# Performance work log

Measured on AMD Instinct MI355X. Metric: run time of the kernel, lower is better.

The kernel has to match this reference:

```python
import jax, jax.numpy as jnp
import numpy as np

E, T, DIN, DOUT = 8, 32768, 1024, 4096


def setup_inputs() -> dict:
    key = jax.random.key(0)
    k1, k2, k3 = jax.random.split(key, 3)
    input = jax.random.normal(k1, (T, DIN), dtype=jnp.float32)
    weight = jax.random.normal(k2, (E, DOUT, DIN), dtype=jnp.float32) * 0.02
    bias = jax.random.normal(k3, (E, DOUT), dtype=jnp.float32) * 0.02
    # balanced routing: 4096 tokens per expert, sums to T
    num_experts_per_token = jnp.full((E,), T // E, dtype=jnp.int64)
    return {"input": input, "weight": weight, "bias": bias,
            "num_experts_per_token": num_experts_per_token}


def reference(input, weight, bias, num_experts_per_token):
    # counts are routing metadata -> static (mirrors .tolist() in torch)
    counts = np.asarray(num_experts_per_token)
    offsets = np.concatenate([[0], np.cumsum(counts)])  # [E+1]
    num_experts = weight.shape[0]
    outs = []
    for i in range(num_experts):  # fixed small loop over experts (grouped GEMM)
        xi = input[offsets[i]:offsets[i + 1]]          # [n_i, DIN]
        yi = xi @ weight[i].T + bias[i]                # [n_i, DOUT]
        outs.append(yi)
    return jnp.concatenate(outs, axis=0)               # [T, DOUT]
```

## Files before the change

kernel.cpp:

```cpp
#include <hip/hip_runtime.h>
#include <hip/hip_bf16.h>


#define DEVFN __device__ __forceinline__

constexpr int E_    = 8;
constexpr int T_    = 32768;
constexpr int DIN_  = 1024;
constexpr int DOUT_ = 4096;

typedef __attribute__((ext_vector_type(8))) __bf16 bf16x8;
typedef __attribute__((ext_vector_type(4))) float  f32x4;
typedef __attribute__((ext_vector_type(8))) short  s16x8;

DEVFN unsigned short f2bf(float x) {
  unsigned u = __builtin_bit_cast(unsigned, x);
  u += 0x7fffu + ((u >> 16) & 1u);
  return (unsigned short)(u >> 16);
}

DEVFN long long expert_offset(const void* cnts, int e) {
  const int* c32 = (const int*)cnts;
  long long s = 0;
  for (int i = 0; i < E_; ++i) s += c32[i];
  if (s == (long long)T_) {
    long long o = 0;
    for (int i = 0; i < e; ++i) o += c32[i];
    return o;
  }
  const long long* c64 = (const long long*)cnts;
  long long o = 0;
  for (int i = 0; i < e; ++i) o += c64[i];
  return o;
}

__global__ __launch_bounds__(256) void cvt2_kernel(const float* __restrict__ ia,
                                                   const float* __restrict__ iw,
                                                   unsigned short* __restrict__ oa,
                                                   unsigned short* __restrict__ ow,
                                                   int nA4, int nW4) {
  int i = blockIdx.x * 256 + threadIdx.x;
  const float* src;
  unsigned short* dst;
  int j;
  if (i < nA4) { src = ia; dst = oa; j = i; }
  else         { j = i - nA4; if (j >= nW4) return; src = iw; dst = ow; }
  const float4 f = reinterpret_cast<const float4*>(src)[j];
  ushort4 h;
  h.x = f2bf(f.x); h.y = f2bf(f.y); h.z = f2bf(f.z); h.w = f2bf(f.w);
  reinterpret_cast<ushort4*>(dst)[j] = h;
}

__global__ __launch_bounds__(512, 2) void gemm5_kernel(const unsigned short* __restrict__ wa,
                                                       const unsigned short* __restrict__ wb,
                                                       const float* __restrict__ bias,
                                                       const void* __restrict__ counts,
                                                       float* __restrict__ out) {
  __shared__ __align__(16) unsigned char lds[2][2][32768];

  const int tid  = threadIdx.x;
  const int lane = tid & 63;
  const int wid  = tid >> 6;
  const int wm = wid >> 2, wn = wid & 3;

  const int p = blockIdx.x;
  const int e = p & 7;
  const int q = p >> 3;

  const long long off = expert_offset(counts, e);
  const unsigned short* wae = wa + off * (long long)DIN_;
  const unsigned short* wbe = wb + (long long)e * DOUT_ * DIN_;
  const float* be = bias + e * DOUT_;

  int goff[4];
#pragma unroll
  for (int rd = 0; rd < 4; ++rd) {
    const int chunk = rd * 512 + tid;
    const int r = chunk >> 3, c = chunk & 7;
    goff[rd] = r * DIN_ + ((c ^ (r & 7)) << 3);
  }
  auto stage = [&](const unsigned short* g, unsigned char* l) {
#pragma unroll
    for (int rd = 0; rd < 4; ++rd)
      __builtin_amdgcn_global_load_lds(
          (const __attribute__((address_space(1))) void*)(g + goff[rd]),
          (__attribute__((address_space(3))) void*)(l + (rd * 512 + tid) * 16), 16, 0, 0);
  };

  const int rsel = lane & 15, hi = lane >> 4;
  int lp[2];
  lp[0] = rsel * 128 + (((hi)     ^ (rsel & 7)) << 4);
  lp[1] = rsel * 128 + (((4 + hi) ^ (rsel & 7)) << 4);
  const int abase = wm * 128 * 128;
  const int bbase = wn * 64 * 128;

  bf16x8 a[4][2];
  bf16x8 b[2][2][2];
  f32x4  acc[8][4];

  auto quad = [&](int am0, int qn) {
#pragma unroll
    for (int mf = 0; mf < 4; ++mf)
#pragma unroll
      for (int j = 0; j < 2; ++j)
#pragma unroll
        for (int kk = 0; kk < 2; ++kk)
          acc[am0 + mf][qn * 2 + j] = __builtin_amdgcn_mfma_f32_16x16x32_bf16(
              a[mf][kk], b[qn][j][kk], acc[am0 + mf][qn * 2 + j], 0, 0, 0);
  };

  int tm = q >> 3, tn = q & 7;
  const unsigned short* wat = wae + (long long)tm * 256 * DIN_;
  const unsigned short* wbt = wbe + (long long)tn * 256 * DIN_;
  stage(wat,      &lds[0][0][0]);
  stage(wbt,      &lds[0][1][0]);
  stage(wat + 64, &lds[1][0][0]);
  stage(wbt + 64, &lds[1][1][0]);
  asm volatile("s_waitcnt vmcnt(8)" ::: "memory");
  __builtin_amdgcn_s_barrier();

  for (int it = 0; it < 8; ++it) {
    const int ocol0 = tn * 256 + wn * 64;
    {
      const float bv0 = be[ocol0 + rsel];
      const float bv1 = be[ocol0 + 16 + rsel];
      const float bv2 = be[ocol0 + 32 + rsel];
      const float bv3 = be[ocol0 + 48 + rsel];
#pragma unroll
      for (int am = 0; am < 8; ++am) {
        acc[am][0] = (f32x4){bv0, bv0, bv0, bv0};
        acc[am][1] = (f32x4){bv1, bv1, bv1, bv1};
        acc[am][2] = (f32x4){bv2, bv2, bv2, bv2};
        acc[am][3] = (f32x4){bv3, bv3, bv3, bv3};
      }
    }
    const bool have_next = (it < 7);
    int ntm = tm, ntn = tn;
    if (have_next) { ntm = ((it + 1) & 3) * 4 + (q >> 3); ntn = ((it + 1) >> 2) * 8 + (q & 7); }
    const unsigned short* nat = wae + (long long)ntm * 256 * DIN_;
    const unsigned short* nbt = wbe + (long long)ntn * 256 * DIN_;

    for (int kt = 0; kt < 16; ++kt) {
      unsigned char* Ab = &lds[kt & 1][0][0];
      unsigned char* Bb = &lds[kt & 1][1][0];
      const unsigned short* pfa = nullptr;
      const unsigned short* pfb = nullptr;
      int nend = -1;
      if (kt < 14)        { pfa = wat + (kt + 2) * 64; pfb = wbt + (kt + 2) * 64; nend = 8; }
      else if (have_next) { pfa = nat + (kt - 14) * 64; pfb = nbt + (kt - 14) * 64; nend = 8; }
      else if (kt == 14)  { nend = 0; }

#pragma unroll
      for (int mf = 0; mf < 4; ++mf) {
        a[mf][0] = *(const bf16x8*)(Ab + abase + mf * 2048 + lp[0]);
        a[mf][1] = *(const bf16x8*)(Ab + abase + mf * 2048 + lp[1]);
      }
#pragma unroll
      for (int j = 0; j < 2; ++j) {
        b[0][j][0] = *(const bf16x8*)(Bb + bbase + j * 2048 + lp[0]);
        b[0][j][1] = *(const bf16x8*)(Bb + bbase + j * 2048 + lp[1]);
      }
      __builtin_amdgcn_s_setprio(1); quad(0, 0); __builtin_amdgcn_s_setprio(0);
#pragma unroll
      for (int j = 0; j < 2; ++j) {
        b[1][j][0] = *(const bf16x8*)(Bb + bbase + 4096 + j * 2048 + lp[0]);
        b[1][j][1] = *(const bf16x8*)(Bb + bbase + 4096 + j * 2048 + lp[1]);
      }
      __builtin_amdgcn_s_setprio(1); quad(0, 1); __builtin_amdgcn_s_setprio(0);
#pragma unroll
      for (int mf = 0; mf < 4; ++mf) {
        a[mf][0] = *(const bf16x8*)(Ab + abase + 8192 + mf * 2048 + lp[0]);
        a[mf][1] = *(const bf16x8*)(Ab + abase + 8192 + mf * 2048 + lp[1]);
      }
      __builtin_amdgcn_s_setprio(1); quad(4, 1); __builtin_amdgcn_s_setprio(0);
      __builtin_amdgcn_s_barrier();

      if (pfb) stage(pfb, Bb);
      if (pfa) stage(pfa, Ab);
      __builtin_amdgcn_sched_barrier(0);
      __builtin_amdgcn_s_setprio(1); quad(4, 0); __builtin_amdgcn_s_setprio(0);
      if (nend == 8)      asm volatile("s_waitcnt vmcnt(8)" ::: "memory");
      else if (nend == 0) asm volatile("s_waitcnt vmcnt(0)" ::: "memory");
      __builtin_amdgcn_s_barrier();
    }

    const long long orow0 = off + (long long)tm * 256 + wm * 128;
#pragma unroll
    for (int am = 0; am < 8; ++am) {
      const int rl = (am >> 2) * 64 + (am & 3) * 16 + hi * 4;
#pragma unroll
      for (int j = 0; j < 4; ++j) {
        float* rp = out + (orow0 + rl + j) * (long long)DOUT_ + ocol0 + rsel;
        rp[0]  = acc[am][0][j];
        rp[16] = acc[am][1][j];
        rp[32] = acc[am][2][j];
        rp[48] = acc[am][3][j];
      }
    }
    wat = nat; wbt = nbt; tm = ntm; tn = ntn;
  }
}

__global__ __launch_bounds__(256) void gemm_fb_kernel(const float* __restrict__ Af,
                                                      const float* __restrict__ Bf,
                                                      const float* __restrict__ bias,
                                                      const void* __restrict__ counts,
                                                      float* __restrict__ out) {
  constexpr int RS = 144;
  constexpr int BBASE = 128 * RS;
  __shared__ __align__(16) unsigned char lds[2 * 128 * RS];

  const int tid  = threadIdx.x;
  const int lane = tid & 63;
  const int wid  = tid >> 6;
  const int wm = wid >> 1, wn = wid & 1;

  const int bid = blockIdx.x;
  const int e  = bid >> 10;
  const int t  = bid & 1023;
  const int tm = t >> 5, tn = t & 31;

  const long long off = expert_offset(counts, e);
  const long long rowA0 = off + (long long)tm * 128;
  const int n0 = tn * 128;

  f32x4 acc[4][4] = {};

  for (int kt = 0; kt < DIN_ / 64; ++kt) {
    const int k0 = kt * 64;
#pragma unroll
    for (int rd = 0; rd < 8; ++rd) {
      const int chunk = rd * 256 + tid;
      const int c2 = chunk & 1023;
      const int r  = c2 >> 3;
      const int c  = c2 & 7;
      const float* src =
          (rd < 4) ? (Af + (rowA0 + r) * (long long)DIN_ + (k0 + c * 8))
                   : (Bf + ((long long)(e * DOUT_ + n0 + r)) * DIN_ + (k0 + c * 8));
      const float4 f0 = *reinterpret_cast<const float4*>(src);
      const float4 f1 = *reinterpret_cast<const float4*>(src + 4);
      s16x8 v;
      v[0] = (short)f2bf(f0.x); v[1] = (short)f2bf(f0.y);
      v[2] = (short)f2bf(f0.z); v[3] = (short)f2bf(f0.w);
      v[4] = (short)f2bf(f1.x); v[5] = (short)f2bf(f1.y);
      v[6] = (short)f2bf(f1.z); v[7] = (short)f2bf(f1.w);
      *reinterpret_cast<s16x8*>(&lds[((rd < 4) ? 0 : BBASE) + r * RS + (c << 4)]) = v;
    }
    __syncthreads();
#pragma unroll
    for (int kk = 0; kk < 2; ++kk) {
      const int rs = lane & 15;
      const int cs = kk * 4 + (lane >> 4);
      bf16x8 af[4], bfr[4];
#pragma unroll
      for (int mf = 0; mf < 4; ++mf)
        af[mf] = *reinterpret_cast<const bf16x8*>(&lds[(wm * 64 + mf * 16 + rs) * RS + (cs << 4)]);
#pragma unroll
      for (int nf = 0; nf < 4; ++nf)
        bfr[nf] = *reinterpret_cast<const bf16x8*>(&lds[BBASE + (wn * 64 + nf * 16 + rs) * RS + (cs << 4)]);
#pragma unroll
      for (int mf = 0; mf < 4; ++mf)
#pragma unroll
        for (int nf = 0; nf < 4; ++nf)
          acc[mf][nf] = __builtin_amdgcn_mfma_f32_16x16x32_bf16(af[mf], bfr[nf], acc[mf][nf], 0, 0, 0);
    }
    __syncthreads();
  }

  const long long orow0 = off + (long long)tm * 128 + wm * 64;
  const int ocol0 = n0 + wn * 64;
  const int rlo = (lane >> 4) * 4;
  const int c15 = lane & 15;
#pragma unroll
  for (int nf = 0; nf < 4; ++nf) {
    const int n = ocol0 + nf * 16 + c15;
    const float bv = bias[e * DOUT_ + n];
#pragma unroll
    for (int mf = 0; mf < 4; ++mf) {
      const long long mrow = orow0 + mf * 16 + rlo;
#pragma unroll
      for (int j = 0; j < 4; ++j)
        out[(mrow + j) * (long long)DOUT_ + n] = acc[mf][nf][j] + bv;
    }
  }
}

extern "C" void kernel_launch(void* const* d_in, const int* in_sizes, int n_in,
                              void* d_out, int out_size, void* d_ws, size_t ws_size,
                              hipStream_t stream) {
  const float* input  = (const float*)d_in[0];
  const float* weight = (const float*)d_in[1];
  const float* bias   = (const float*)d_in[2];
  const void*  counts = (const void*)d_in[3];
  float* out = (float*)d_out;

  const size_t nA = (size_t)T_ * DIN_;
  const size_t nW = (size_t)E_ * DOUT_ * DIN_;
  const size_t need = (nA + nW) * sizeof(unsigned short);

  if (ws_size >= need) {
    unsigned short* wa = (unsigned short*)d_ws;
    unsigned short* wb = wa + nA;
    const int nA4 = (int)(nA / 4), nW4 = (int)(nW / 4);
    cvt2_kernel<<<dim3((unsigned)((nA4 + nW4) / 256)), dim3(256), 0, stream>>>(
        input, weight, wa, wb, nA4, nW4);
    gemm5_kernel<<<dim3(256), dim3(512), 0, stream>>>(wa, wb, bias, counts, out);
  } else {
    gemm_fb_kernel<<<dim3(E_ * 32 * 32), dim3(256), 0, stream>>>(input, weight, bias, counts, out);
  }
}
```

Before: 385.6 us.

## Load B fragments directly from global memory instead of staging through LDS

The weight (B) tile is no longer staged into shared memory. Each lane now loads its MFMA B fragments straight from global memory, and only the A tile is double-buffered through LDS. This halves LDS usage and staging traffic per block, which could allow more occupancy and fewer LDS reads. The cost is that B loads now go uncoalesced across lanes, hitting a 16-row by 16-byte pattern, and each B element is re-read by the two wm warps. These loads also sit on the critical path with no prefetch, and the vmcnt waits now count these extra loads, which may add stalls.

Measured after the change: 550.5 us. 42.8% more time.

```diff
diff --git a/kernel.cpp b/kernel.cpp
--- a/kernel.cpp
+++ b/kernel.cpp
@@ -51,12 +51,12 @@
   reinterpret_cast<ushort4*>(dst)[j] = h;
 }
 
-__global__ __launch_bounds__(512, 2) void gemm5_kernel(const unsigned short* __restrict__ wa,
+__global__ __launch_bounds__(512, 2) void gemm6_kernel(const unsigned short* __restrict__ wa,
                                                        const unsigned short* __restrict__ wb,
                                                        const float* __restrict__ bias,
                                                        const void* __restrict__ counts,
                                                        float* __restrict__ out) {
-  __shared__ __align__(16) unsigned char lds[2][2][32768];
+  __shared__ __align__(16) unsigned char lds[2][32768];
 
   const int tid  = threadIdx.x;
   const int lane = tid & 63;
@@ -79,7 +79,7 @@
     const int r = chunk >> 3, c = chunk & 7;
     goff[rd] = r * DIN_ + ((c ^ (r & 7)) << 3);
   }
-  auto stage = [&](const unsigned short* g, unsigned char* l) {
+  auto stageA = [&](const unsigned short* g, unsigned char* l) {
 #pragma unroll
     for (int rd = 0; rd < 4; ++rd)
       __builtin_amdgcn_global_load_lds(
@@ -92,7 +92,6 @@
   lp[0] = rsel * 128 + (((hi)     ^ (rsel & 7)) << 4);
   lp[1] = rsel * 128 + (((4 + hi) ^ (rsel & 7)) << 4);
   const int abase = wm * 128 * 128;
-  const int bbase = wn * 64 * 128;
 
   bf16x8 a[4][2];
   bf16x8 b[2][2][2];
@@ -112,15 +111,19 @@
   int tm = q >> 3, tn = q & 7;
   const unsigned short* wat = wae + (long long)tm * 256 * DIN_;
   const unsigned short* wbt = wbe + (long long)tn * 256 * DIN_;
-  stage(wat,      &lds[0][0][0]);
-  stage(wbt,      &lds[0][1][0]);
-  stage(wat + 64, &lds[1][0][0]);
-  stage(wbt + 64, &lds[1][1][0]);
-  asm volatile("s_waitcnt vmcnt(8)" ::: "memory");
+  stageA(wat,      &lds[0][0]);
+  stageA(wat + 64, &lds[1][0]);
+  asm volatile("s_waitcnt vmcnt(4)" ::: "memory");
   __builtin_amdgcn_s_barrier();
 
   for (int it = 0; it < 8; ++it) {
     const int ocol0 = tn * 256 + wn * 64;
+    const unsigned short* bptr[2][2];
+#pragma unroll
+    for (int nq = 0; nq < 2; ++nq)
+#pragma unroll
+      for (int j = 0; j < 2; ++j)
+        bptr[nq][j] = wbt + (long long)(wn * 64 + nq * 32 + j * 16 + rsel) * DIN_ + hi * 8;
     {
       const float bv0 = be[ocol0 + rsel];
       const float bv1 = be[ocol0 + 16 + rsel];
@@ -141,31 +144,26 @@
     const unsigned short* nbt = wbe + (long long)ntn * 256 * DIN_;
 
     for (int kt = 0; kt < 16; ++kt) {
-      unsigned char* Ab = &lds[kt & 1][0][0];
-      unsigned char* Bb = &lds[kt & 1][1][0];
+      unsigned char* Ab = &lds[kt & 1][0];
       const unsigned short* pfa = nullptr;
-      const unsigned short* pfb = nullptr;
       int nend = -1;
-      if (kt < 14)        { pfa = wat + (kt + 2) * 64; pfb = wbt + (kt + 2) * 64; nend = 8; }
-      else if (have_next) { pfa = nat + (kt - 14) * 64; pfb = nbt + (kt - 14) * 64; nend = 8; }
+      if (kt < 14)        { pfa = wat + (kt + 2) * 64; nend = 4; }
+      else if (have_next) { pfa = nat + (kt - 14) * 64; nend = 4; }
       else if (kt == 14)  { nend = 0; }
 
+#pragma unroll
+      for (int nq = 0; nq < 2; ++nq)
+#pragma unroll
+        for (int j = 0; j < 2; ++j)
+#pragma unroll
+          for (int kk = 0; kk < 2; ++kk)
+            b[nq][j][kk] = *(const bf16x8*)(bptr[nq][j] + kt * 64 + kk * 32);
 #pragma unroll
       for (int mf = 0; mf < 4; ++mf) {
         a[mf][0] = *(const bf16x8*)(Ab + abase + mf * 2048 + lp[0]);
         a[mf][1] = *(const bf16x8*)(Ab + abase + mf * 2048 + lp[1]);
       }
-#pragma unroll
-      for (int j = 0; j < 2; ++j) {
-        b[0][j][0] = *(const bf16x8*)(Bb + bbase + j * 2048 + lp[0]);
-        b[0][j][1] = *(const bf16x8*)(Bb + bbase + j * 2048 + lp[1]);
-      }
       __builtin_amdgcn_s_setprio(1); quad(0, 0); __builtin_amdgcn_s_setprio(0);
-#pragma unroll
-      for (int j = 0; j < 2; ++j) {
-        b[1][j][0] = *(const bf16x8*)(Bb + bbase + 4096 + j * 2048 + lp[0]);
-        b[1][j][1] = *(const bf16x8*)(Bb + bbase + 4096 + j * 2048 + lp[1]);
-      }
       __builtin_amdgcn_s_setprio(1); quad(0, 1); __builtin_amdgcn_s_setprio(0);
 #pragma unroll
       for (int mf = 0; mf < 4; ++mf) {
@@ -175,11 +173,10 @@
       __builtin_amdgcn_s_setprio(1); quad(4, 1); __builtin_amdgcn_s_setprio(0);
       __builtin_amdgcn_s_barrier();
 
-      if (pfb) stage(pfb, Bb);
-      if (pfa) stage(pfa, Ab);
+      if (pfa) stageA(pfa, Ab);
       __builtin_amdgcn_sched_barrier(0);
       __builtin_amdgcn_s_setprio(1); quad(4, 0); __builtin_amdgcn_s_setprio(0);
-      if (nend == 8)      asm volatile("s_waitcnt vmcnt(8)" ::: "memory");
+      if (nend == 4)      asm volatile("s_waitcnt vmcnt(4)" ::: "memory");
       else if (nend == 0) asm volatile("s_waitcnt vmcnt(0)" ::: "memory");
       __builtin_amdgcn_s_barrier();
     }
@@ -304,7 +301,7 @@
     const int nA4 = (int)(nA / 4), nW4 = (int)(nW / 4);
     cvt2_kernel<<<dim3((unsigned)((nA4 + nW4) / 256)), dim3(256), 0, stream>>>(
         input, weight, wa, wb, nA4, nW4);
-    gemm5_kernel<<<dim3(256), dim3(512), 0, stream>>>(wa, wb, bias, counts, out);
+    gemm6_kernel<<<dim3(256), dim3(512), 0, stream>>>(wa, wb, bias, counts, out);
   } else {
     gemm_fb_kernel<<<dim3(E_ * 32 * 32), dim3(256), 0, stream>>>(input, weight, bias, counts, out);
   }
```

## Software-pipeline the MFMA quadrants across k-steps with double register fragments

Applied to the files above, without the earlier changes.

Splits the A and B register fragments into two sets so that one quadrant of MFMAs from the previous k-step (4,1) runs while the next k-step's LDS fragments are being read. The remaining three quadrants then issue back to back, and the deferred quadrant is drained after the k-loop. The aim is to hide LDS read latency behind matrix work and remove the mid-loop MFMA that used to sit after the barrier. In exchange it raises register pressure from the duplicated fragment arrays, which could cause spills under the 512x2 launch bounds. It also adds an explicit lgkmcnt wait before the barrier.

New measurement: 410.7 us. 6.5% more time.

```diff
diff --git a/kernel.cpp b/kernel.cpp
--- a/kernel.cpp
+++ b/kernel.cpp
@@ -51,7 +51,7 @@
   reinterpret_cast<ushort4*>(dst)[j] = h;
 }
 
-__global__ __launch_bounds__(512, 2) void gemm5_kernel(const unsigned short* __restrict__ wa,
+__global__ __launch_bounds__(512, 2) void gemm7_kernel(const unsigned short* __restrict__ wa,
                                                        const unsigned short* __restrict__ wb,
                                                        const float* __restrict__ bias,
                                                        const void* __restrict__ counts,
@@ -94,11 +94,11 @@
   const int abase = wm * 128 * 128;
   const int bbase = wn * 64 * 128;
 
-  bf16x8 a[4][2];
-  bf16x8 b[2][2][2];
+  bf16x8 a0r[4][2], a1r[4][2];
+  bf16x8 b0r[2][2], b1r[2][2];
   f32x4  acc[8][4];
 
-  auto quad = [&](int am0, int qn) {
+  auto quad = [&](int am0, int qn, bf16x8 (&A)[4][2], bf16x8 (&B)[2][2]) {
 #pragma unroll
     for (int mf = 0; mf < 4; ++mf)
 #pragma unroll
@@ -106,7 +106,7 @@
 #pragma unroll
         for (int kk = 0; kk < 2; ++kk)
           acc[am0 + mf][qn * 2 + j] = __builtin_amdgcn_mfma_f32_16x16x32_bf16(
-              a[mf][kk], b[qn][j][kk], acc[am0 + mf][qn * 2 + j], 0, 0, 0);
+              A[mf][kk], B[j][kk], acc[am0 + mf][qn * 2 + j], 0, 0, 0);
   };
 
   int tm = q >> 3, tn = q & 7;
@@ -151,38 +151,48 @@
       else if (kt == 14)  { nend = 0; }
 
 #pragma unroll
+      for (int j = 0; j < 2; ++j) {
+        b0r[j][0] = *(const bf16x8*)(Bb + bbase + j * 2048 + lp[0]);
+        b0r[j][1] = *(const bf16x8*)(Bb + bbase + j * 2048 + lp[1]);
+      }
+#pragma unroll
       for (int mf = 0; mf < 4; ++mf) {
-        a[mf][0] = *(const bf16x8*)(Ab + abase + mf * 2048 + lp[0]);
-        a[mf][1] = *(const bf16x8*)(Ab + abase + mf * 2048 + lp[1]);
+        a0r[mf][0] = *(const bf16x8*)(Ab + abase + mf * 2048 + lp[0]);
+        a0r[mf][1] = *(const bf16x8*)(Ab + abase + mf * 2048 + lp[1]);
+      }
+      if (kt > 0) {
+        __builtin_amdgcn_s_setprio(1);
+        quad(4, 1, a1r, b1r);
+        __builtin_amdgcn_s_setprio(0);
+      }
+#pragma unroll
+      for (int mf = 0; mf < 4; ++mf) {
+        a1r[mf][0] = *(const bf16x8*)(Ab + abase + 8192 + mf * 2048 + lp[0]);
+        a1r[mf][1] = *(const bf16x8*)(Ab + abase + 8192 + mf * 2048 + lp[1]);
       }
 #pragma unroll
       for (int j = 0; j < 2; ++j) {
-        b[0][j][0] = *(const bf16x8*)(Bb + bbase + j * 2048 + lp[0]);
-        b[0][j][1] = *(const bf16x8*)(Bb + bbase + j * 2048 + lp[1]);
-      }
-      __builtin_amdgcn_s_setprio(1); quad(0, 0); __builtin_amdgcn_s_setprio(0);
-#pragma unroll
-      for (int j = 0; j < 2; ++j) {
-        b[1][j][0] = *(const bf16x8*)(Bb + bbase + 4096 + j * 2048 + lp[0]);
-        b[1][j][1] = *(const bf16x8*)(Bb + bbase + 4096 + j * 2048 + lp[1]);
-      }
-      __builtin_amdgcn_s_setprio(1); quad(0, 1); __builtin_amdgcn_s_setprio(0);
-#pragma unroll
-      for (int mf = 0; mf < 4; ++mf) {
-        a[mf][0] = *(const bf16x8*)(Ab + abase + 8192 + mf * 2048 + lp[0]);
-        a[mf][1] = *(const bf16x8*)(Ab + abase + 8192 + mf * 2048 + lp[1]);
-      }
-      __builtin_amdgcn_s_setprio(1); quad(4, 1); __builtin_amdgcn_s_setprio(0);
+        b1r[j][0] = *(const bf16x8*)(Bb + bbase + 4096 + j * 2048 + lp[0]);
+        b1r[j][1] = *(const bf16x8*)(Bb + bbase + 4096 + j * 2048 + lp[1]);
+      }
+      __builtin_amdgcn_s_setprio(1);
+      quad(0, 0, a0r, b0r);
+      quad(0, 1, a0r, b1r);
+      quad(4, 0, a1r, b0r);
+      __builtin_amdgcn_s_setprio(0);
+      asm volatile("s_waitcnt lgkmcnt(0)" ::: "memory");
       __builtin_amdgcn_s_barrier();
 
       if (pfb) stage(pfb, Bb);
       if (pfa) stage(pfa, Ab);
-      __builtin_amdgcn_sched_barrier(0);
-      __builtin_amdgcn_s_setprio(1); quad(4, 0); __builtin_amdgcn_s_setprio(0);
       if (nend == 8)      asm volatile("s_waitcnt vmcnt(8)" ::: "memory");
       else if (nend == 0) asm volatile("s_waitcnt vmcnt(0)" ::: "memory");
       __builtin_amdgcn_s_barrier();
     }
+
+    __builtin_amdgcn_s_setprio(1);
+    quad(4, 1, a1r, b1r);
+    __builtin_amdgcn_s_setprio(0);
 
     const long long orow0 = off + (long long)tm * 256 + wm * 128;
 #pragma unroll
@@ -304,7 +314,7 @@
     const int nA4 = (int)(nA / 4), nW4 = (int)(nW / 4);
     cvt2_kernel<<<dim3((unsigned)((nA4 + nW4) / 256)), dim3(256), 0, stream>>>(
         input, weight, wa, wb, nA4, nW4);
-    gemm5_kernel<<<dim3(256), dim3(512), 0, stream>>>(wa, wb, bias, counts, out);
+    gemm7_kernel<<<dim3(256), dim3(512), 0, stream>>>(wa, wb, bias, counts, out);
   } else {
     gemm_fb_kernel<<<dim3(E_ * 32 * 32), dim3(256), 0, stream>>>(input, weight, bias, counts, out);
   }
```
